# Kernel optimization log

Hardware: AMD Instinct MI355X
Metric: run time of the kernel (lower is better)

## Reference

```python
import jax, jax.numpy as jnp
import numpy as np

N, D_IN, D_OUT = 8192, 1024, 1024

def setup_inputs() -> dict:
    key = jax.random.key(0)
    kx, kq, kk, kv = jax.random.split(key, 4)
    s = 1.0 / np.sqrt(D_IN)
    return {
        "x": jax.random.normal(kx, (N, D_IN), dtype=jnp.float32),
        "W_q": jax.random.normal(kq, (D_OUT, D_IN), dtype=jnp.float32) * s,
        "W_k": jax.random.normal(kk, (D_OUT, D_IN), dtype=jnp.float32) * s,
        "W_v": jax.random.normal(kv, (D_OUT, D_IN), dtype=jnp.float32) * s,
    }

def reference(x, W_q, W_k, W_v):
    # nn.Linear stores weight as [out, in]: y = x @ W.T
    q = x @ W_q.T          # [N, D_OUT]
    k = x @ W_k.T          # [N, D_OUT]
    v = x @ W_v.T          # [N, D_OUT]
    scale = 1.0 / jnp.sqrt(jnp.asarray(k.shape[-1], dtype=x.dtype))
    scores = (q @ k.T) * scale            # [N, N]
    attn = jax.nn.softmax(scores, axis=-1)
    return attn @ v                        # [N, D_OUT]
```

## Files before the change

### kernel.cpp

```cpp
#include <hip/hip_runtime.h>
#include <hip/hip_bf16.h>
#include <cstdint>
#include <cstddef>


typedef __attribute__((ext_vector_type(8))) short short8;
typedef __attribute__((ext_vector_type(8))) unsigned short ushort8;
typedef __attribute__((ext_vector_type(4))) float f32x4;

__device__ __forceinline__ unsigned short f2bf(float f) {
  unsigned u = __float_as_uint(f);
  u += 0x7fffu + ((u >> 16) & 1u);
  return (unsigned short)(u >> 16);
}
__device__ __forceinline__ float bf2f(unsigned short h) {
  return __uint_as_float(((unsigned)h) << 16);
}

__device__ __forceinline__ void glds16(const void* g, void* l) {
  __builtin_amdgcn_global_load_lds((__attribute__((address_space(1))) void*)g,
                                   (__attribute__((address_space(3))) void*)l,
                                   16, 0, 0);
}

__global__ __launch_bounds__(256) void cast_kernel(const float* __restrict__ in,
                                                   unsigned short* __restrict__ out,
                                                   int n8) {
  int i = blockIdx.x * 256 + threadIdx.x;
  if (i >= n8) return;
  const f32x4* in4 = (const f32x4*)in;
  f32x4 a = in4[2 * i];
  f32x4 b = in4[2 * i + 1];
  ushort8 o;
#pragma unroll
  for (int j = 0; j < 4; ++j) o[j] = f2bf(a[j]);
#pragma unroll
  for (int j = 0; j < 4; ++j) o[4 + j] = f2bf(b[j]);
  ((ushort8*)out)[i] = o;
}

#define BM 128
#define BN 128
#define BKK 32

template <typename OutT>
__global__ __launch_bounds__(256, 2) void gemm_bt(
    const unsigned short* __restrict__ A, const unsigned short* __restrict__ B,
    OutT* __restrict__ C, int M, int N, int K, float scale) {
  __shared__ unsigned short As[BM * BKK];
  __shared__ unsigned short Bs[BN * BKK];

  const int t = threadIdx.x;
  const int lane = t & 63, w = t >> 6;
  const int wr = w >> 1, wc = w & 1;
  const int lrow = lane & 15, kgrp = lane >> 4;
  const int bm = blockIdx.y, bn = blockIdx.x;

  f32x4 acc[4][4];
#pragma unroll
  for (int m = 0; m < 4; ++m)
#pragma unroll
    for (int n = 0; n < 4; ++n) acc[m][n] = (f32x4)(0.0f);

  const int o0 = w * 1024 + lane * 16;
  const int o1 = o0 + 4096;
  const int r0 = o0 >> 6, c0 = o0 & 63;
  const int r1 = o1 >> 6, c1 = o1 & 63;

  const size_t ldab = (size_t)K * 2;
  const char* Abase = (const char*)A + (size_t)bm * BM * ldab;
  const char* Bbase = (const char*)B + (size_t)bn * BN * ldab;
  char* AsB = (char*)As;
  char* BsB = (char*)Bs;

  for (int kt = 0; kt < K; kt += BKK) {
    __syncthreads();
    glds16(Abase + (size_t)r0 * ldab + (size_t)kt * 2 + c0, AsB + w * 1024);
    glds16(Abase + (size_t)r1 * ldab + (size_t)kt * 2 + c1, AsB + 4096 + w * 1024);
    glds16(Bbase + (size_t)r0 * ldab + (size_t)kt * 2 + c0, BsB + w * 1024);
    glds16(Bbase + (size_t)r1 * ldab + (size_t)kt * 2 + c1, BsB + 4096 + w * 1024);
    __syncthreads();

    short8 aF[4], bF[4];
#pragma unroll
    for (int m = 0; m < 4; ++m)
      aF[m] = *(const short8*)&As[(wr * 64 + m * 16 + lrow) * BKK + kgrp * 8];
#pragma unroll
    for (int n = 0; n < 4; ++n)
      bF[n] = *(const short8*)&Bs[(wc * 64 + n * 16 + lrow) * BKK + kgrp * 8];
#pragma unroll
    for (int m = 0; m < 4; ++m)
#pragma unroll
      for (int n = 0; n < 4; ++n)
        acc[m][n] = __builtin_amdgcn_mfma_f32_16x16x32_bf16(aF[m], bF[n],
                                                            acc[m][n], 0, 0, 0);
  }

  const int crow = bm * BM + wr * 64;
  const int ccol = bn * BN + wc * 64;
#pragma unroll
  for (int m = 0; m < 4; ++m) {
#pragma unroll
    for (int n = 0; n < 4; ++n) {
      int r = crow + m * 16 + kgrp * 4;
      int c = ccol + n * 16 + lrow;
      f32x4 v = acc[m][n];
#pragma unroll
      for (int j = 0; j < 4; ++j) {
        float val = v[j] * scale;
        if (sizeof(OutT) == 2) {
          ((unsigned short*)C)[(size_t)(r + j) * N + c] = f2bf(val);
        } else {
          ((float*)C)[(size_t)(r + j) * N + c] = val;
        }
      }
    }
  }
}

__global__ __launch_bounds__(256) void softmax_kernel(unsigned short* __restrict__ S,
                                                      int ncol) {
  const int t = threadIdx.x;
  unsigned short* rp = S + (size_t)blockIdx.x * ncol;
  ushort8* rv = (ushort8*)rp;
  const int nch = ncol >> 11;
  float f[32];
#pragma unroll
  for (int c = 0; c < 4; ++c) {
    if (c < nch) {
      ushort8 v = rv[c * 256 + t];
#pragma unroll
      for (int j = 0; j < 8; ++j) f[c * 8 + j] = bf2f(v[j]);
    }
  }
  float m = -1e30f;
#pragma unroll
  for (int i = 0; i < 32; ++i) m = fmaxf(m, f[i]);
#pragma unroll
  for (int o = 32; o; o >>= 1) m = fmaxf(m, __shfl_xor(m, o));
  __shared__ float red[8];
  if ((t & 63) == 0) red[t >> 6] = m;
  __syncthreads();
  m = fmaxf(fmaxf(red[0], red[1]), fmaxf(red[2], red[3]));

  float s = 0.0f;
#pragma unroll
  for (int i = 0; i < 32; ++i) {
    f[i] = __expf(f[i] - m);
    s += f[i];
  }
#pragma unroll
  for (int o = 32; o; o >>= 1) s += __shfl_xor(s, o);
  if ((t & 63) == 0) red[4 + (t >> 6)] = s;
  __syncthreads();
  s = red[4] + red[5] + red[6] + red[7];
  float inv = 1.0f / s;
#pragma unroll
  for (int c = 0; c < 4; ++c) {
    if (c < nch) {
      ushort8 v;
#pragma unroll
      for (int j = 0; j < 8; ++j) v[j] = f2bf(f[c * 8 + j] * inv);
      rv[c * 256 + t] = v;
    }
  }
}

__global__ __launch_bounds__(256) void transpose_kernel(
    const unsigned short* __restrict__ in, unsigned short* __restrict__ out,
    int R, int Ccols) {
  __shared__ unsigned short tile[64][65];
  const int tx = threadIdx.x & 63, ty = threadIdx.x >> 6;
  const int r0 = blockIdx.y * 64, c0 = blockIdx.x * 64;
#pragma unroll
  for (int i = 0; i < 16; ++i) {
    int r = ty * 16 + i;
    tile[r][tx] = in[(size_t)(r0 + r) * Ccols + c0 + tx];
  }
  __syncthreads();
#pragma unroll
  for (int i = 0; i < 16; ++i) {
    int r = ty * 16 + i;
    out[(size_t)(c0 + r) * R + r0 + tx] = tile[tx][r];
  }
}

extern "C" void kernel_launch(void* const* d_in, const int* in_sizes, int n_in,
                              void* d_out, int out_size, void* d_ws, size_t ws_size,
                              hipStream_t stream) {
  (void)in_sizes; (void)n_in; (void)out_size; (void)ws_size;
  const int N = 8192, D = 1024;
  const float* x  = (const float*)d_in[0];
  const float* Wq = (const float*)d_in[1];
  const float* Wk = (const float*)d_in[2];
  const float* Wv = (const float*)d_in[3];
  float* out = (float*)d_out;

  char* ws = (char*)d_ws;
  size_t off = 0;
  auto alloc = [&](size_t bytes) { char* p = ws + off; off += bytes; return p; };
  unsigned short* xh  = (unsigned short*)alloc((size_t)N * D * 2);
  unsigned short* Wqh = (unsigned short*)alloc((size_t)D * D * 2);
  unsigned short* Wkh = (unsigned short*)alloc((size_t)D * D * 2);
  unsigned short* Wvh = (unsigned short*)alloc((size_t)D * D * 2);
  unsigned short* Qh  = (unsigned short*)alloc((size_t)N * D * 2);
  unsigned short* Kh  = (unsigned short*)alloc((size_t)N * D * 2);
  unsigned short* Vh  = (unsigned short*)alloc((size_t)N * D * 2);
  unsigned short* S   = (unsigned short*)alloc((size_t)N * N * 2);
  unsigned short* Vth = xh;

  cast_kernel<<<(N * D / 8) / 256, 256, 0, stream>>>(x, xh, N * D / 8);
  cast_kernel<<<(D * D / 8) / 256, 256, 0, stream>>>(Wq, Wqh, D * D / 8);
  cast_kernel<<<(D * D / 8) / 256, 256, 0, stream>>>(Wk, Wkh, D * D / 8);
  cast_kernel<<<(D * D / 8) / 256, 256, 0, stream>>>(Wv, Wvh, D * D / 8);

  dim3 gqkv(D / BN, N / BM);
  gemm_bt<unsigned short><<<gqkv, 256, 0, stream>>>(xh, Wqh, Qh, N, D, D, 1.0f);
  gemm_bt<unsigned short><<<gqkv, 256, 0, stream>>>(xh, Wkh, Kh, N, D, D, 1.0f);
  gemm_bt<unsigned short><<<gqkv, 256, 0, stream>>>(xh, Wvh, Vh, N, D, D, 1.0f);

  dim3 gs(N / BN, N / BM);
  gemm_bt<unsigned short><<<gs, 256, 0, stream>>>(Qh, Kh, S, N, N, D, 0.03125f);

  softmax_kernel<<<N, 256, 0, stream>>>(S, N);

  transpose_kernel<<<dim3(D / 64, N / 64), 256, 0, stream>>>(Vh, Vth, N, D);

  dim3 go(D / BN, N / BM);
  gemm_bt<float><<<go, 256, 0, stream>>>(S, Vth, out, N, D, N, 1.0f);
}
```

Baseline: 623.1 us.

## Replace GEMM with 256x256 tiled, 4-stage pipelined, swizzled MFMA kernel

```diff
diff --git a/kernel.cpp b/kernel.cpp
--- a/kernel.cpp
+++ b/kernel.cpp
@@ -7,6 +7,8 @@
 typedef __attribute__((ext_vector_type(8))) short short8;
 typedef __attribute__((ext_vector_type(8))) unsigned short ushort8;
 typedef __attribute__((ext_vector_type(4))) float f32x4;
+
+#define FENCE asm volatile("" ::: "memory")
 
 __device__ __forceinline__ unsigned short f2bf(float f) {
   unsigned u = __float_as_uint(f);
@@ -39,82 +41,184 @@
   ((ushort8*)out)[i] = o;
 }
 
-#define BM 128
-#define BN 128
-#define BKK 32
+#define MFMA_OP(mi, ni, av, bv) \
+  acc[mi][ni] = __builtin_amdgcn_mfma_f32_16x16x32_bf16(av, bv, acc[mi][ni], 0, 0, 0)
 
 template <typename OutT>
-__global__ __launch_bounds__(256, 2) void gemm_bt(
+__device__ __forceinline__ void gemm_core(
     const unsigned short* __restrict__ A, const unsigned short* __restrict__ B,
-    OutT* __restrict__ C, int M, int N, int K, float scale) {
-  __shared__ unsigned short As[BM * BKK];
-  __shared__ unsigned short Bs[BN * BKK];
-
-  const int t = threadIdx.x;
-  const int lane = t & 63, w = t >> 6;
-  const int wr = w >> 1, wc = w & 1;
-  const int lrow = lane & 15, kgrp = lane >> 4;
-  const int bm = blockIdx.y, bn = blockIdx.x;
-
-  f32x4 acc[4][4];
-#pragma unroll
-  for (int m = 0; m < 4; ++m)
+    OutT* __restrict__ C, int ldc, size_t ldab , int NT,
+    int gm0, int gn0, float scale, char* lA, char* lB) {
+  const int tid = threadIdx.x;
+  const int lane = tid & 63, w = tid >> 6;
+  const int wm = w >> 2, wn = w & 3;
+
+  const int rc0 = w * 32 + (lane >> 2);
+  const int rc1 = rc0 + 16;
+  const int scol = ((lane & 3) << 4) ^ (((lane >> 3) & 3) << 4);
+  const char* pA0 = (const char*)A + (size_t)(gm0 + rc0) * ldab + scol;
+  const char* pA1 = (const char*)A + (size_t)(gm0 + rc1) * ldab + scol;
+  const char* pB0 = (const char*)B + (size_t)(gn0 + rc0) * ldab + scol;
+  const char* pB1 = (const char*)B + (size_t)(gn0 + rc1) * ldab + scol;
+  char* dA = lA + w * 2048;
+  char* dB = lB + w * 2048;
+
+  const int colb = ((lane >> 4) << 4) ^ (((lane >> 1) & 3) << 4);
+  const int aoff = (wm * 128 + (lane & 15)) * 64 + colb;
+  const int boff = (wn * 64 + (lane & 15)) * 64 + colb;
+
+  f32x4 acc[8][4];
+#pragma unroll
+  for (int m = 0; m < 8; ++m)
 #pragma unroll
     for (int n = 0; n < 4; ++n) acc[m][n] = (f32x4)(0.0f);
 
-  const int o0 = w * 1024 + lane * 16;
-  const int o1 = o0 + 4096;
-  const int r0 = o0 >> 6, c0 = o0 & 63;
-  const int r1 = o1 >> 6, c1 = o1 & 63;
-
-  const size_t ldab = (size_t)K * 2;
-  const char* Abase = (const char*)A + (size_t)bm * BM * ldab;
-  const char* Bbase = (const char*)B + (size_t)bn * BN * ldab;
-  char* AsB = (char*)As;
-  char* BsB = (char*)Bs;
-
-  for (int kt = 0; kt < K; kt += BKK) {
-    __syncthreads();
-    glds16(Abase + (size_t)r0 * ldab + (size_t)kt * 2 + c0, AsB + w * 1024);
-    glds16(Abase + (size_t)r1 * ldab + (size_t)kt * 2 + c1, AsB + 4096 + w * 1024);
-    glds16(Bbase + (size_t)r0 * ldab + (size_t)kt * 2 + c0, BsB + w * 1024);
-    glds16(Bbase + (size_t)r1 * ldab + (size_t)kt * 2 + c1, BsB + 4096 + w * 1024);
-    __syncthreads();
-
-    short8 aF[4], bF[4];
-#pragma unroll
-    for (int m = 0; m < 4; ++m)
-      aF[m] = *(const short8*)&As[(wr * 64 + m * 16 + lrow) * BKK + kgrp * 8];
-#pragma unroll
-    for (int n = 0; n < 4; ++n)
-      bF[n] = *(const short8*)&Bs[(wc * 64 + n * 16 + lrow) * BKK + kgrp * 8];
-#pragma unroll
-    for (int m = 0; m < 4; ++m)
-#pragma unroll
-      for (int n = 0; n < 4; ++n)
-        acc[m][n] = __builtin_amdgcn_mfma_f32_16x16x32_bf16(aF[m], bF[n],
-                                                            acc[m][n], 0, 0, 0);
-  }
-
-  const int crow = bm * BM + wr * 64;
-  const int ccol = bn * BN + wc * 64;
-#pragma unroll
-  for (int m = 0; m < 4; ++m) {
-#pragma unroll
-    for (int n = 0; n < 4; ++n) {
-      int r = crow + m * 16 + kgrp * 4;
-      int c = ccol + n * 16 + lrow;
-      f32x4 v = acc[m][n];
+  for (int t = 0; t < 2; ++t) {
+    glds16(pA0 + (size_t)t * 64, dA + t * 16384);
+    glds16(pA1 + (size_t)t * 64, dA + t * 16384 + 1024);
+    glds16(pB0 + (size_t)t * 64, dB + t * 16384);
+    glds16(pB1 + (size_t)t * 64, dB + t * 16384 + 1024);
+  }
+  asm volatile("s_waitcnt vmcnt(4)" ::: "memory");
+  __builtin_amdgcn_s_barrier();
+  FENCE;
+
+  for (int t = 0; t < NT; ++t) {
+    const int slot = t & 3;
+    const char* As = lA + slot * 16384;
+    const char* Bs = lB + slot * 16384;
+    const bool stg = (t + 2 < NT);
+    const int s2 = (t + 2) & 3;
+    const size_t go = (size_t)(t + 2) * 64;
+    short8 a0, a1, a2, a3, b0, b1, b2, b3;
+
+    if (stg) glds16(pA0 + go, dA + s2 * 16384);
+    a0 = *(const short8*)(As + aoff);
+    a1 = *(const short8*)(As + aoff + 1024);
+    a2 = *(const short8*)(As + aoff + 2048);
+    a3 = *(const short8*)(As + aoff + 3072);
+    b0 = *(const short8*)(Bs + boff);
+    b1 = *(const short8*)(Bs + boff + 1024);
+    __builtin_amdgcn_s_setprio(1);
+    MFMA_OP(0, 0, a0, b0); MFMA_OP(0, 1, a0, b1);
+    MFMA_OP(1, 0, a1, b0); MFMA_OP(1, 1, a1, b1);
+    MFMA_OP(2, 0, a2, b0); MFMA_OP(2, 1, a2, b1);
+    MFMA_OP(3, 0, a3, b0); MFMA_OP(3, 1, a3, b1);
+    __builtin_amdgcn_s_setprio(0);
+    FENCE; __builtin_amdgcn_s_barrier(); FENCE;
+
+    if (stg) glds16(pA1 + go, dA + s2 * 16384 + 1024);
+    b2 = *(const short8*)(Bs + boff + 2048);
+    b3 = *(const short8*)(Bs + boff + 3072);
+    __builtin_amdgcn_s_setprio(1);
+    MFMA_OP(0, 2, a0, b2); MFMA_OP(0, 3, a0, b3);
+    MFMA_OP(1, 2, a1, b2); MFMA_OP(1, 3, a1, b3);
+    MFMA_OP(2, 2, a2, b2); MFMA_OP(2, 3, a2, b3);
+    MFMA_OP(3, 2, a3, b2); MFMA_OP(3, 3, a3, b3);
+    __builtin_amdgcn_s_setprio(0);
+    FENCE; __builtin_amdgcn_s_barrier(); FENCE;
+
+    if (stg) glds16(pB0 + go, dB + s2 * 16384);
+    a0 = *(const short8*)(As + aoff + 4096);
+    a1 = *(const short8*)(As + aoff + 5120);
+    a2 = *(const short8*)(As + aoff + 6144);
+    a3 = *(const short8*)(As + aoff + 7168);
+    __builtin_amdgcn_s_setprio(1);
+    MFMA_OP(4, 0, a0, b0); MFMA_OP(4, 1, a0, b1);
+    MFMA_OP(5, 0, a1, b0); MFMA_OP(5, 1, a1, b1);
+    MFMA_OP(6, 0, a2, b0); MFMA_OP(6, 1, a2, b1);
+    MFMA_OP(7, 0, a3, b0); MFMA_OP(7, 1, a3, b1);
+    __builtin_amdgcn_s_setprio(0);
+    FENCE; __builtin_amdgcn_s_barrier(); FENCE;
+
+    if (stg) glds16(pB1 + go, dB + s2 * 16384 + 1024);
+    __builtin_amdgcn_s_setprio(1);
+    MFMA_OP(4, 2, a0, b2); MFMA_OP(4, 3, a0, b3);
+    MFMA_OP(5, 2, a1, b2); MFMA_OP(5, 3, a1, b3);
+    MFMA_OP(6, 2, a2, b2); MFMA_OP(6, 3, a2, b3);
+    MFMA_OP(7, 2, a3, b2); MFMA_OP(7, 3, a3, b3);
+    __builtin_amdgcn_s_setprio(0);
+    if (stg) asm volatile("s_waitcnt vmcnt(4)" ::: "memory");
+    else     asm volatile("s_waitcnt vmcnt(0)" ::: "memory");
+    __builtin_amdgcn_s_barrier();
+    FENCE;
+  }
+
+  const int r0 = gm0 + wm * 128 + ((lane >> 4) << 2);
+  const int c0 = gn0 + wn * 64 + (lane & 15);
+#pragma unroll
+  for (int mi = 0; mi < 8; ++mi) {
+#pragma unroll
+    for (int ni = 0; ni < 4; ++ni) {
+      f32x4 v = acc[mi][ni];
 #pragma unroll
       for (int j = 0; j < 4; ++j) {
         float val = v[j] * scale;
-        if (sizeof(OutT) == 2) {
-          ((unsigned short*)C)[(size_t)(r + j) * N + c] = f2bf(val);
-        } else {
-          ((float*)C)[(size_t)(r + j) * N + c] = val;
-        }
+        size_t idx = (size_t)(r0 + mi * 16 + j) * ldc + (c0 + ni * 16);
+        if (sizeof(OutT) == 2) ((unsigned short*)C)[idx] = f2bf(val);
+        else                   ((float*)C)[idx] = val;
       }
     }
+  }
+}
+
+__device__ __forceinline__ void swz_block(int& bx, int& by, int& bz) {
+  const int gx = gridDim.x, gy = gridDim.y;
+  const int f = (blockIdx.z * gy + blockIdx.y) * gx + blockIdx.x;
+  const int nwg = gx * gy * gridDim.z;
+  const int q = nwg >> 3;
+  const int l = (f & 7) * q + (f >> 3);
+  bx = l % gx;
+  const int r = l / gx;
+  by = r % gy;
+  bz = r / gy;
+}
+
+__global__ __launch_bounds__(512, 2) void gemm_s_kernel(
+    const unsigned short* __restrict__ Q, const unsigned short* __restrict__ Kh,
+    unsigned short* __restrict__ S) {
+  __shared__ char lA[4 * 16384];
+  __shared__ char lB[4 * 16384];
+  int bx, by, bz; swz_block(bx, by, bz);
+  gemm_core<unsigned short>(Q, Kh, S, 8192, 2048, 32, by * 256, bx * 256,
+                            0.03125f, lA, lB);
+}
+
+__global__ __launch_bounds__(512, 2) void gemm_qkv_kernel(
+    const unsigned short* __restrict__ X,
+    const unsigned short* __restrict__ Wq, const unsigned short* __restrict__ Wk,
+    const unsigned short* __restrict__ Wv,
+    unsigned short* __restrict__ Qo, unsigned short* __restrict__ Ko,
+    unsigned short* __restrict__ Vo) {
+  __shared__ char lA[4 * 16384];
+  __shared__ char lB[4 * 16384];
+  int bx, by, bz; swz_block(bx, by, bz);
+  const unsigned short* B = (bz == 0) ? Wq : (bz == 1) ? Wk : Wv;
+  unsigned short* C = (bz == 0) ? Qo : (bz == 1) ? Ko : Vo;
+  gemm_core<unsigned short>(X, B, C, 1024, 2048, 32, by * 256, bx * 256,
+                            1.0f, lA, lB);
+}
+
+__global__ __launch_bounds__(512, 2) void gemm_pv_kernel(
+    const unsigned short* __restrict__ S, const unsigned short* __restrict__ Vt,
+    float* __restrict__ O, float* __restrict__ P1) {
+  __shared__ char lA[4 * 16384];
+  __shared__ char lB[4 * 16384];
+  int bx, by, bz; swz_block(bx, by, bz);
+  const unsigned short* A = S + (size_t)bz * 4096;
+  const unsigned short* B = Vt + (size_t)bz * 4096;
+  float* C = bz ? P1 : O;
+  gemm_core<float>(A, B, C, 1024, 16384, 128, by * 256, bx * 256, 1.0f, lA, lB);
+}
+
+__global__ __launch_bounds__(256) void add_kernel(float* __restrict__ out,
+                                                  const float* __restrict__ p,
+                                                  int n4) {
+  int i = blockIdx.x * 256 + threadIdx.x;
+  if (i < n4) {
+    f32x4 a = ((const f32x4*)out)[i];
+    f32x4 b = ((const f32x4*)p)[i];
+    ((f32x4*)out)[i] = a + b;
   }
 }
 
@@ -123,15 +227,12 @@
   const int t = threadIdx.x;
   unsigned short* rp = S + (size_t)blockIdx.x * ncol;
   ushort8* rv = (ushort8*)rp;
-  const int nch = ncol >> 11;
   float f[32];
 #pragma unroll
   for (int c = 0; c < 4; ++c) {
-    if (c < nch) {
-      ushort8 v = rv[c * 256 + t];
-#pragma unroll
-      for (int j = 0; j < 8; ++j) f[c * 8 + j] = bf2f(v[j]);
-    }
+    ushort8 v = rv[c * 256 + t];
+#pragma unroll
+    for (int j = 0; j < 8; ++j) f[c * 8 + j] = bf2f(v[j]);
   }
   float m = -1e30f;
 #pragma unroll
@@ -157,12 +258,10 @@
   float inv = 1.0f / s;
 #pragma unroll
   for (int c = 0; c < 4; ++c) {
-    if (c < nch) {
-      ushort8 v;
-#pragma unroll
-      for (int j = 0; j < 8; ++j) v[j] = f2bf(f[c * 8 + j] * inv);
-      rv[c * 256 + t] = v;
-    }
+    ushort8 v;
+#pragma unroll
+    for (int j = 0; j < 8; ++j) v[j] = f2bf(f[c * 8 + j] * inv);
+    rv[c * 256 + t] = v;
   }
 }
 
@@ -208,24 +307,23 @@
   unsigned short* Vh  = (unsigned short*)alloc((size_t)N * D * 2);
   unsigned short* S   = (unsigned short*)alloc((size_t)N * N * 2);
   unsigned short* Vth = xh;
+  float* Pbuf = (float*)Qh;
 
   cast_kernel<<<(N * D / 8) / 256, 256, 0, stream>>>(x, xh, N * D / 8);
   cast_kernel<<<(D * D / 8) / 256, 256, 0, stream>>>(Wq, Wqh, D * D / 8);
   cast_kernel<<<(D * D / 8) / 256, 256, 0, stream>>>(Wk, Wkh, D * D / 8);
   cast_kernel<<<(D * D / 8) / 256, 256, 0, stream>>>(Wv, Wvh, D * D / 8);
 
-  dim3 gqkv(D / BN, N / BM);
-  gemm_bt<unsigned short><<<gqkv, 256, 0, stream>>>(xh, Wqh, Qh, N, D, D, 1.0f);
-  gemm_bt<unsigned short><<<gqkv, 256, 0, stream>>>(xh, Wkh, Kh, N, D, D, 1.0f);
-  gemm_bt<unsigned short><<<gqkv, 256, 0, stream>>>(xh, Wvh, Vh, N, D, D, 1.0f);
-
-  dim3 gs(N / BN, N / BM);
-  gemm_bt<unsigned short><<<gs, 256, 0, stream>>>(Qh, Kh, S, N, N, D, 0.03125f);
+  gemm_qkv_kernel<<<dim3(4, 32, 3), 512, 0, stream>>>(xh, Wqh, Wkh, Wvh,
+                                                      Qh, Kh, Vh);
+
+  gemm_s_kernel<<<dim3(32, 32), 512, 0, stream>>>(Qh, Kh, S);
 
   softmax_kernel<<<N, 256, 0, stream>>>(S, N);
 
   transpose_kernel<<<dim3(D / 64, N / 64), 256, 0, stream>>>(Vh, Vth, N, D);
 
-  dim3 go(D / BN, N / BM);
-  gemm_bt<float><<<go, 256, 0, stream>>>(S, Vth, out, N, D, N, 1.0f);
-}
+  gemm_pv_kernel<<<dim3(4, 32, 2), 512, 0, stream>>>(S, Vth, out, Pbuf);
+
+  add_kernel<<<(N * D / 4) / 256, 256, 0, stream>>>(out, Pbuf, N * D / 4);
+}
```

After: 608.9 us. -2.3%, faster.
